# Kernel optimization log

Hardware: AMD Instinct MI355X
Metric: run time of the kernel (lower is better)

The kernel has to match this reference:

```python
import jax, jax.numpy as jnp
import numpy as np

B, S, H, NH = 2, 2048, 1024, 16
D = H // NH
EPS = 1.1920929e-07  # torch fp32 finfo eps used by F.rms_norm default
ROPE_BASE = 10000.0


def setup_inputs() -> dict:
    key = jax.random.key(0)
    k0, k1, k2, k3 = jax.random.split(key, 4)
    return {
        "x": jax.random.normal(k0, (B, S, H), jnp.float32),
        "ve": jax.random.normal(k1, (B, S, H), jnp.float32),
        "W_qkv": jax.random.normal(k2, (3 * H, H), jnp.float32) * 0.02,
        "W_o": jax.random.normal(k3, (H, H), jnp.float32) * 0.02,
        "lambdas": jnp.array([0.5, 0.5], jnp.float32),
    }


def _rms_norm(x):
    # F.rms_norm without learnable weight, over last dim
    return x * jax.lax.rsqrt(jnp.mean(x * x, axis=-1, keepdims=True) + EPS)


def _rope(x):
    # x: [b, s, h, d]; rotate-half style RoPE matching the Rotary module
    d = x.shape[-1]
    inv_freq = (1.0 / ROPE_BASE) ** (jnp.arange(0, d, 2, dtype=jnp.float32) / d)
    t = jnp.arange(x.shape[1], dtype=jnp.float32)
    freqs = t[:, None] * inv_freq[None, :]          # [s, d/2]
    cos = jnp.cos(freqs)[None, :, None, :]
    sin = jnp.sin(freqs)[None, :, None, :]
    x1, x2 = jnp.split(x, 2, axis=-1)
    return jnp.concatenate([x1 * cos + x2 * sin, -x1 * sin + x2 * cos], axis=-1)


def reference(x, ve, W_qkv, W_o, lambdas):
    qkv = x @ W_qkv.T                                # [b, s, 3H]
    q, k, v = jnp.split(qkv, 3, axis=-1)
    rs = lambda a: a.reshape(B, S, NH, D)            # b s (h d) -> b s h d
    q, k, v = rs(q), rs(k), rs(v)
    q = _rope(_rms_norm(q))
    k = _rope(_rms_norm(k))
    v = lambdas[0] * v + lambdas[1] * rs(ve)         # value-lambda mix
    scale = 1.0 / jnp.sqrt(jnp.asarray(D, jnp.float32))  # flex_attention default
    scores = jnp.einsum('bqhd,bkhd->bhqk', q, k) * scale
    causal = jnp.tril(jnp.ones((S, S), bool))
    scores = jnp.where(causal[None, None], scores, jnp.asarray(-jnp.inf, scores.dtype))
    p = jax.nn.softmax(scores, axis=-1)
    a = jnp.einsum('bhqk,bkhd->bqhd', p, v).reshape(B, S, H)
    return a @ W_o.T
```

## Files before the change

kernel.cpp:

```cpp
#include <hip/hip_runtime.h>
#include <math.h>

typedef __bf16 bf16;
typedef __attribute__((ext_vector_type(8))) __bf16 bf16x8;
typedef __attribute__((ext_vector_type(4))) __bf16 bf16x4;
typedef __attribute__((ext_vector_type(4))) float f32x4;

#define B_  2
#define S_  2048
#define H_  1024
#define NH_ 16
#define D_  64

__device__ __forceinline__ f32x4 mfma16(bf16x8 a, bf16x8 b, f32x4 c) {
    return __builtin_amdgcn_mfma_f32_16x16x32_bf16(a, b, c, 0, 0, 0);
}

__device__ __forceinline__ void async16(void* lds, const void* g) {
    __builtin_amdgcn_global_load_lds(
        (const __attribute__((address_space(1))) unsigned int*)g,
        (__attribute__((address_space(3))) unsigned int*)lds, 16, 0, 0);
}

__global__ __launch_bounds__(256) void cvt_main(
    const float* __restrict__ x, const float* __restrict__ wqkv,
    bf16* __restrict__ xb, bf16* __restrict__ wqb, float2* __restrict__ tab)
{
    const int bid = blockIdx.x, tid = threadIdx.x;
    if (bid < 4096) {
        int i = bid * 256 + tid;
        f32x4 v = *(const f32x4*)(x + (size_t)i * 4);
        bf16x4 o; o[0]=(bf16)v[0]; o[1]=(bf16)v[1]; o[2]=(bf16)v[2]; o[3]=(bf16)v[3];
        *(bf16x4*)(xb + (size_t)i * 4) = o;
    } else if (bid < 7168) {
        int i = (bid - 4096) * 256 + tid;
        f32x4 v = *(const f32x4*)(wqkv + (size_t)i * 4);
        bf16x4 o; o[0]=(bf16)v[0]; o[1]=(bf16)v[1]; o[2]=(bf16)v[2]; o[3]=(bf16)v[3];
        *(bf16x4*)(wqb + (size_t)i * 4) = o;
    } else {
        int idx = (bid - 7168) * 256 + tid;
        int s = idx >> 5, i = idx & 31;
        float f = exp2f((float)i * (-13.287712379549449f / 32.0f));
        float sn, cs;
        sincosf((float)s * f, &sn, &cs);
        tab[idx] = make_float2(cs, sn);
    }
}

__global__ __launch_bounds__(256) void cvt_bf16(const float* __restrict__ src,
                                                bf16* __restrict__ dst, int n4) {
    int i = blockIdx.x * 256 + threadIdx.x;
    if (i >= n4) return;
    f32x4 v = *(const f32x4*)(src + (size_t)i * 4);
    bf16x4 o; o[0]=(bf16)v[0]; o[1]=(bf16)v[1]; o[2]=(bf16)v[2]; o[3]=(bf16)v[3];
    *(bf16x4*)(dst + (size_t)i * 4) = o;
}

__global__ __launch_bounds__(512, 2) void gemm_qkv(
    const bf16* __restrict__ A, const bf16* __restrict__ W,
    bf16* __restrict__ qb, bf16* __restrict__ kb, bf16* __restrict__ vtb,
    const float* __restrict__ ve, const float* __restrict__ lambdas,
    const float2* __restrict__ tab)
{
    constexpr int K  = H_;
    constexpr int NS = K >> 6;
    __shared__ bf16 Al[2][256][64];
    __shared__ bf16 Bl[2][256][64];
    const int id = blockIdx.x + 12 * blockIdx.y;
    const int rX = id & 7, qX = id >> 3;
    const int m0 = ((rX >> 2) * 8 + qX / 3) * 256;
    const int n0 = ((rX & 3) * 3 + qX % 3) * 256;
    const int tid  = threadIdx.x;
    const int lane = tid & 63;
    const int w    = tid >> 6;
    const int quad = lane >> 4;
    const int l16  = lane & 15;
    const int l7r  = l16 & 7;
    const int wm   = (w >> 2) * 128;
    const int wn   = (w & 3) * 64;
    const int r8   = lane >> 3;
    const int cs   = ((lane & 7) ^ r8) * 8;

    auto stage_half = [&](int sl, int kt, int h) {
        const int k0 = kt << 6;
        if (h < 2) {
            const bf16* g = A + (size_t)(m0 + h * 128 + w * 16 + r8) * K + k0 + cs;
            async16(&Al[sl][h * 128 + w * 16][0],     g);
            async16(&Al[sl][h * 128 + w * 16 + 8][0], g + (size_t)8 * K);
        } else {
            const bf16* g = W + (size_t)(n0 + (h - 2) * 128 + w * 16 + r8) * K + k0 + cs;
            async16(&Bl[sl][(h - 2) * 128 + w * 16][0],     g);
            async16(&Bl[sl][(h - 2) * 128 + w * 16 + 8][0], g + (size_t)8 * K);
        }
    };

    const f32x4 Z4 = {0.f, 0.f, 0.f, 0.f};
    f32x4 acc[8][4];
#pragma unroll
    for (int i = 0; i < 8; ++i)
#pragma unroll
        for (int j = 0; j < 4; ++j) acc[i][j] = Z4;

    stage_half(0, 0, 0); stage_half(0, 0, 1); stage_half(0, 0, 2); stage_half(0, 0, 3);
    stage_half(1, (NS > 1 ? 1 : 0), 0);

    for (int t = 0; t < NS; ++t) {
        const int cur = t & 1;
        const int kt1 = (t + 1 < NS) ? t + 1 : NS - 1;
        const int kt2 = (t + 2 < NS) ? t + 2 : NS - 1;
        bf16x8 aL[4][2], aH[4][2], bq0[2][2], bq1[2][2];

        asm volatile("s_waitcnt vmcnt(2)" ::: "memory");
        __builtin_amdgcn_s_barrier();
#pragma unroll
        for (int ks = 0; ks < 2; ++ks) {
#pragma unroll
            for (int i = 0; i < 4; ++i)
                aL[i][ks] = *(const bf16x8*)
                    &Al[cur][wm + i * 16 + l16][(((ks << 2) + quad) ^ l7r) * 8];
#pragma unroll
            for (int j = 0; j < 2; ++j)
                bq0[j][ks] = *(const bf16x8*)
                    &Bl[cur][wn + j * 16 + l16][(((ks << 2) + quad) ^ l7r) * 8];
        }
        stage_half(cur ^ 1, kt1, 1);
        __builtin_amdgcn_s_setprio(1);
#pragma unroll
        for (int ks = 0; ks < 2; ++ks)
#pragma unroll
            for (int i = 0; i < 4; ++i)
#pragma unroll
                for (int j = 0; j < 2; ++j)
                    acc[i][j] = mfma16(aL[i][ks], bq0[j][ks], acc[i][j]);
        __builtin_amdgcn_s_setprio(0);

        __builtin_amdgcn_s_barrier();
#pragma unroll
        for (int ks = 0; ks < 2; ++ks)
#pragma unroll
            for (int j = 0; j < 2; ++j)
                bq1[j][ks] = *(const bf16x8*)
                    &Bl[cur][wn + 32 + j * 16 + l16][(((ks << 2) + quad) ^ l7r) * 8];
        stage_half(cur ^ 1, kt1, 2);
        __builtin_amdgcn_s_setprio(1);
#pragma unroll
        for (int ks = 0; ks < 2; ++ks)
#pragma unroll
            for (int i = 0; i < 4; ++i)
#pragma unroll
                for (int j = 0; j < 2; ++j)
                    acc[i][2 + j] = mfma16(aL[i][ks], bq1[j][ks], acc[i][2 + j]);
        __builtin_amdgcn_s_setprio(0);

        __builtin_amdgcn_s_barrier();
#pragma unroll
        for (int ks = 0; ks < 2; ++ks)
#pragma unroll
            for (int i = 0; i < 4; ++i)
                aH[i][ks] = *(const bf16x8*)
                    &Al[cur][wm + 64 + i * 16 + l16][(((ks << 2) + quad) ^ l7r) * 8];
        stage_half(cur ^ 1, kt1, 3);
        __builtin_amdgcn_s_setprio(1);
#pragma unroll
        for (int ks = 0; ks < 2; ++ks)
#pragma unroll
            for (int i = 0; i < 4; ++i)
#pragma unroll
                for (int j = 0; j < 2; ++j)
                    acc[4 + i][j] = mfma16(aH[i][ks], bq0[j][ks], acc[4 + i][j]);
        __builtin_amdgcn_s_setprio(0);

        __builtin_amdgcn_s_barrier();
        stage_half(cur, kt2, 0);
        __builtin_amdgcn_s_setprio(1);
#pragma unroll
        for (int ks = 0; ks < 2; ++ks)
#pragma unroll
            for (int i = 0; i < 4; ++i)
#pragma unroll
                for (int j = 0; j < 2; ++j)
                    acc[4 + i][2 + j] = mfma16(aH[i][ks], bq1[j][ks], acc[4 + i][2 + j]);
        __builtin_amdgcn_s_setprio(0);
    }
    asm volatile("s_waitcnt vmcnt(0)" ::: "memory");

    const int nbase = n0 + wn;
    const int which = nbase >> 10;
    const int h     = (nbase & (H_ - 1)) >> 6;
    if (which < 2) {
        bf16* dst = which ? kb : qb;
#pragma unroll
        for (int i = 0; i < 8; ++i) {
            float ss[4];
#pragma unroll
            for (int r = 0; r < 4; ++r)
                ss[r] = acc[i][0][r] * acc[i][0][r] + acc[i][1][r] * acc[i][1][r]
                      + acc[i][2][r] * acc[i][2][r] + acc[i][3][r] * acc[i][3][r];
#pragma unroll
            for (int r = 0; r < 4; ++r) {
                ss[r] += __shfl_xor(ss[r], 1);
                ss[r] += __shfl_xor(ss[r], 2);
                ss[r] += __shfl_xor(ss[r], 4);
                ss[r] += __shfl_xor(ss[r], 8);
            }
#pragma unroll
            for (int r = 0; r < 4; ++r) {
                int    m   = m0 + wm + i * 16 + quad * 4 + r;
                int    bb  = m >> 11, s = m & (S_ - 1);
                float  rms = rsqrtf(ss[r] * (1.0f / 64.0f) + 1.1920929e-07f);
                float  x0 = acc[i][0][r] * rms, x1 = acc[i][1][r] * rms;
                float  x2 = acc[i][2][r] * rms, x3 = acc[i][3][r] * rms;
                float2 t0 = tab[(size_t)s * 32 + l16];
                float2 t1 = tab[(size_t)s * 32 + 16 + l16];
                bf16*  bp = dst + ((size_t)(bb * NH_ + h) * S_ + s) * D_;
                bp[l16]      = (bf16)(x0 * t0.x + x2 * t0.y);
                bp[16 + l16] = (bf16)(x1 * t1.x + x3 * t1.y);
                bp[32 + l16] = (bf16)(x2 * t0.x - x0 * t0.y);
                bp[48 + l16] = (bf16)(x3 * t1.x - x1 * t1.y);
            }
        }
    } else {
        const float l0 = lambdas[0], l1 = lambdas[1];
#pragma unroll
        for (int i = 0; i < 8; ++i) {
            const int m00 = m0 + wm + i * 16 + quad * 4;
            const int bb  = m00 >> 11, s = m00 & (S_ - 1);
#pragma unroll
            for (int j = 0; j < 4; ++j) {
                const int d = j * 16 + l16;
                bf16x4 pk;
#pragma unroll
                for (int r = 0; r < 4; ++r) {
                    float vm = l0 * acc[i][j][r]
                             + l1 * ve[(size_t)(m00 + r) * H_ + h * 64 + d];
                    pk[r] = (bf16)vm;
                }
                *(bf16x4*)&vtb[((size_t)(bb * NH_ + h) * D_ + d) * S_ + s] = pk;
            }
        }
    }
}

template <int EPI, int NT>
__global__ __launch_bounds__(256) void gemm_bt(
    const bf16* __restrict__ A, const bf16* __restrict__ W,
    int M, int N, int K,
    float* __restrict__ outF)
{
    constexpr int JN = NT / 32;
    __shared__ bf16 Al[128][64];
    __shared__ bf16 Bl[NT][64];
    const int id = blockIdx.x + 16 * blockIdx.y;
    const int rX = id & 7, qX = id >> 3;
    const int m0 = ((rX >> 2) * 16 + (qX >> 2)) * 128;
    const int n0 = ((rX & 3) * 4 + (qX & 3)) * NT;
    const int tid  = threadIdx.x;
    const int lane = tid & 63;
    const int w    = tid >> 6;
    const int quad = lane >> 4;
    const int l16  = lane & 15;
    const int wm   = (w >> 1) * 64;
    const int wn   = (w & 1) * (NT / 2);
    const int r8   = lane >> 3;
    const int cs   = ((lane & 7) ^ r8) * 8;

    const f32x4 Z4 = {0.f, 0.f, 0.f, 0.f};
    f32x4 acc[4][JN];
#pragma unroll
    for (int i = 0; i < 4; ++i)
#pragma unroll
        for (int j = 0; j < JN; ++j) acc[i][j] = Z4;

    for (int k0 = 0; k0 < K; k0 += 64) {
        {
            const bf16* gA = A + (size_t)(m0 + w * 32 + r8) * K + k0 + cs;
            async16(&Al[w * 32][0],      gA);
            async16(&Al[w * 32 + 8][0],  gA + (size_t)8  * K);
            async16(&Al[w * 32 + 16][0], gA + (size_t)16 * K);
            async16(&Al[w * 32 + 24][0], gA + (size_t)24 * K);
        }
        {
            const bf16* gB = W + (size_t)(n0 + w * 16 + r8) * K + k0 + cs;
            async16(&Bl[w * 16][0],     gB);
            async16(&Bl[w * 16 + 8][0], gB + (size_t)8 * K);
        }
        __syncthreads();
#pragma unroll
        for (int ks = 0; ks < 2; ++ks) {
            bf16x8 af[4], bfg[JN];
#pragma unroll
            for (int i = 0; i < 4; ++i)
                af[i] = *(const bf16x8*)
                    &Al[wm + i * 16 + l16][(((ks << 2) + quad) ^ (l16 & 7)) * 8];
#pragma unroll
            for (int j = 0; j < JN; ++j)
                bfg[j] = *(const bf16x8*)
                    &Bl[wn + j * 16 + l16][(((ks << 2) + quad) ^ (l16 & 7)) * 8];
#pragma unroll
            for (int i = 0; i < 4; ++i)
#pragma unroll
                for (int j = 0; j < JN; ++j)
                    acc[i][j] = mfma16(af[i], bfg[j], acc[i][j]);
        }
        __syncthreads();
    }

#pragma unroll
    for (int i = 0; i < 4; ++i)
#pragma unroll
        for (int j = 0; j < JN; ++j)
#pragma unroll
            for (int r = 0; r < 4; ++r) {
                int m = m0 + wm + i * 16 + quad * 4 + r;
                int n = n0 + wn + j * 16 + l16;
                outF[(size_t)m * N + n] = acc[i][j][r];
            }
}

__global__ __launch_bounds__(256) void attn(
    const bf16* __restrict__ Q, const bf16* __restrict__ Kg,
    const bf16* __restrict__ Vt, bf16* __restrict__ Og)
{
    __shared__ bf16 Kl[2][64][64];
    __shared__ bf16 Vl[2][64][64];
    __shared__ bf16 Pl[4][16][64];

    const int id  = blockIdx.x;
    const int xcd = id & 7;
    const int jj  = id >> 3;
    const int sH  = jj & 3;
    const int cC  = jj >> 2;
    const int bh  = xcd + 8 * sH;
    const int c2  = (cC + 16) & 31;
    const int qt  = (sH == 0) ? cC : (sH == 1) ? 31 - cC
                  : (sH == 2) ? c2 : 31 - c2;

    const int b    = bh >> 4;
    const int h    = bh & 15;
    const int tid  = threadIdx.x;
    const int lane = tid & 63;
    const int w    = tid >> 6;
    const int quad = lane >> 4;
    const int l16  = lane & 15;
    const int l7   = l16 & 7;

    const bf16* Qp = Q  + (size_t)bh * S_ * D_;
    const bf16* Kp = Kg + (size_t)bh * S_ * D_;
    const bf16* Vp = Vt + (size_t)bh * D_ * S_;

    const int srow = lane >> 3;
    const int schk = (lane & 7) ^ (lane >> 3);
    const f32x4 Z4 = {0.f, 0.f, 0.f, 0.f};
    const float C1 = 0.18033688011112042f;
    const float C2 = -11.541560327111707f;

    auto stage = [&](int p, int kb0) {
        const bf16* gK = Kp + (size_t)(kb0 + w * 16 + srow) * D_ + schk * 8;
        async16(&Kl[p][w * 16][0], gK);
        async16(&Kl[p][w * 16 + 8][0], gK + (size_t)8 * D_);
        const bf16* gV = Vp + (size_t)(w * 16 + srow) * S_ + kb0 + schk * 8;
        async16(&Vl[p][w * 16][0], gV);
        async16(&Vl[p][w * 16 + 8][0], gV + (size_t)8 * S_);
    };

    const int qbase = qt * 64 + w * 16;
    const int qi    = qbase + l16;

    const bf16x8 qf0 = *(const bf16x8*)(Qp + (size_t)(qbase + l16) * D_ + quad * 8);
    const bf16x8 qf1 = *(const bf16x8*)(Qp + (size_t)(qbase + l16) * D_ + 32 + quad * 8);

    f32x4 of[4];
#pragma unroll
    for (int dt = 0; dt < 4; ++dt) of[dt] = Z4;
    float lsum = 0.f;

    const int nch = qt + 1;
    stage(0, 0);
    for (int c = 0; c < nch; ++c) {
        const int p   = c & 1;
        const int kb0 = c * 64;
        __syncthreads();
        if (c + 1 < nch) stage(p ^ 1, kb0 + 64);

        float ps = 0.f;
        if (c < qt) {
#pragma unroll
            for (int nt = 0; nt < 4; ++nt) {
                bf16x8 kf0 = *(const bf16x8*)&Kl[p][nt * 16 + l16][(quad ^ l7) * 8];
                bf16x8 kf1 = *(const bf16x8*)&Kl[p][nt * 16 + l16][((quad + 4) ^ l7) * 8];
                f32x4 sacc = Z4;
                sacc = mfma16(kf0, qf0, sacc);
                sacc = mfma16(kf1, qf1, sacc);
                bf16x4 pk;
#pragma unroll
                for (int r = 0; r < 4; ++r) {
                    float pv = exp2f(fmaf(sacc[r], C1, C2));
                    ps += pv;
                    pk[r] = (bf16)pv;
                }
                *(bf16x4*)&Pl[w][l16][((nt * 2 + (quad >> 1)) ^ l7) * 8 + (quad & 1) * 4] = pk;
            }
        } else {
#pragma unroll
            for (int nt = 0; nt < 4; ++nt) {
                bf16x8 kf0 = *(const bf16x8*)&Kl[p][nt * 16 + l16][(quad ^ l7) * 8];
                bf16x8 kf1 = *(const bf16x8*)&Kl[p][nt * 16 + l16][((quad + 4) ^ l7) * 8];
                f32x4 sacc = Z4;
                sacc = mfma16(kf0, qf0, sacc);
                sacc = mfma16(kf1, qf1, sacc);
                bf16x4 pk;
#pragma unroll
                for (int r = 0; r < 4; ++r) {
                    int   key = kb0 + nt * 16 + quad * 4 + r;
                    float pv  = (key <= qi) ? exp2f(fmaf(sacc[r], C1, C2)) : 0.f;
                    ps += pv;
                    pk[r] = (bf16)pv;
                }
                *(bf16x4*)&Pl[w][l16][((nt * 2 + (quad >> 1)) ^ l7) * 8 + (quad & 1) * 4] = pk;
            }
        }
        ps += __shfl_xor(ps, 16);
        ps += __shfl_xor(ps, 32);
        lsum += ps;

        bf16x8 pf0 = *(const bf16x8*)&Pl[w][l16][(quad ^ l7) * 8];
        bf16x8 pf1 = *(const bf16x8*)&Pl[w][l16][((quad + 4) ^ l7) * 8];
#pragma unroll
        for (int dt = 0; dt < 4; ++dt) {
            bf16x8 vf0 = *(const bf16x8*)&Vl[p][dt * 16 + l16][(quad ^ l7) * 8];
            bf16x8 vf1 = *(const bf16x8*)&Vl[p][dt * 16 + l16][((quad + 4) ^ l7) * 8];
            of[dt] = mfma16(pf0, vf0, of[dt]);
            of[dt] = mfma16(pf1, vf1, of[dt]);
        }
    }

#pragma unroll
    for (int r = 0; r < 4; ++r) {
        float ld = __shfl(lsum, quad * 4 + r);
        float rl = 1.0f / ld;
        int   qq = qbase + quad * 4 + r;
#pragma unroll
        for (int dt = 0; dt < 4; ++dt)
            Og[((size_t)(b * S_ + qq)) * H_ + h * D_ + dt * 16 + l16] =
                (bf16)(of[dt][r] * rl);
    }
}

extern "C" void kernel_launch(void* const* d_in, const int* in_sizes, int n_in,
                              void* d_out, int out_size, void* d_ws, size_t ws_size,
                              hipStream_t stream)
{
    const float* x       = (const float*)d_in[0];
    const float* ve      = (const float*)d_in[1];
    const float* Wqkv    = (const float*)d_in[2];
    const float* Wo      = (const float*)d_in[3];
    const float* lambdas = (const float*)d_in[4];
    float* out = (float*)d_out;

    char* od = (char*)d_out;
    char* ws = (char*)d_ws;
    const size_t MB = 1024 * 1024;
    bf16*   xb  = (bf16*)(od);
    bf16*   wqb = (bf16*)(od + 8 * MB);
    float2* tab = (float2*)(od + 14 * MB);
    bf16*   qb  = (bf16*)(ws);
    bf16*   kb  = (bf16*)(ws + 8 * MB);
    bf16*   vtb = (bf16*)(ws + 16 * MB);
    bf16*   ao  = (bf16*)(ws + 24 * MB);
    bf16*   wob = (bf16*)(ws);

    cvt_main<<<7424, 256, 0, stream>>>(x, Wqkv, xb, wqb, tab);
    gemm_qkv<<<dim3(12, 16), 512, 0, stream>>>(
        xb, wqb, qb, kb, vtb, ve, lambdas, (const float2*)tab);
    attn<<<dim3(1024), 256, 0, stream>>>(qb, kb, vtb, ao);
    cvt_bf16<<<1024, 256, 0, stream>>>(Wo, wob, (H_ * H_) / 4);
    gemm_bt<1, 64><<<dim3(16, 32), 256, 0, stream>>>(
        ao, wob, B_ * S_, H_, H_, out);
}
```

Baseline: 207.4 us.

## Double-buffer output projection GEMM with async prefetch two stages ahead

Replaces the templated single-buffered output GEMM with a specialized kernel that keeps two LDS stages, prefetching the k-tile two steps ahead while computing the current one. Full __syncthreads pairs become explicit vmcnt waits plus raw barriers, and MFMA sections run under raised wave priority. The goal is to hide global-to-LDS load latency in the final projection. LDS use doubles, and there is a risk from relying on vmcnt counting of the async loads.

```diff
diff --git a/kernel.cpp b/kernel.cpp
--- a/kernel.cpp
+++ b/kernel.cpp
@@ -241,74 +241,93 @@
     }
 }
 
-template <int EPI, int NT>
-__global__ __launch_bounds__(256) void gemm_bt(
+__global__ __launch_bounds__(256) void gemm_o(
     const bf16* __restrict__ A, const bf16* __restrict__ W,
-    int M, int N, int K,
     float* __restrict__ outF)
 {
-    constexpr int JN = NT / 32;
-    __shared__ bf16 Al[128][64];
-    __shared__ bf16 Bl[NT][64];
+    constexpr int K  = H_;
+    constexpr int N  = H_;
+    constexpr int NS = K >> 6;
+    __shared__ bf16 Al[2][128][64];
+    __shared__ bf16 Bl[2][64][64];
     const int id = blockIdx.x + 16 * blockIdx.y;
     const int rX = id & 7, qX = id >> 3;
     const int m0 = ((rX >> 2) * 16 + (qX >> 2)) * 128;
-    const int n0 = ((rX & 3) * 4 + (qX & 3)) * NT;
+    const int n0 = ((rX & 3) * 4 + (qX & 3)) * 64;
     const int tid  = threadIdx.x;
     const int lane = tid & 63;
     const int w    = tid >> 6;
     const int quad = lane >> 4;
     const int l16  = lane & 15;
+    const int l7r  = l16 & 7;
     const int wm   = (w >> 1) * 64;
-    const int wn   = (w & 1) * (NT / 2);
+    const int wn   = (w & 1) * 32;
     const int r8   = lane >> 3;
     const int cs   = ((lane & 7) ^ r8) * 8;
 
+    auto stage = [&](int sl, int k0) {
+        const bf16* gA = A + (size_t)(m0 + w * 32 + r8) * K + k0 + cs;
+        async16(&Al[sl][w * 32][0],      gA);
+        async16(&Al[sl][w * 32 + 8][0],  gA + (size_t)8  * K);
+        async16(&Al[sl][w * 32 + 16][0], gA + (size_t)16 * K);
+        async16(&Al[sl][w * 32 + 24][0], gA + (size_t)24 * K);
+        const bf16* gB = W + (size_t)(n0 + w * 16 + r8) * K + k0 + cs;
+        async16(&Bl[sl][w * 16][0],     gB);
+        async16(&Bl[sl][w * 16 + 8][0], gB + (size_t)8 * K);
+    };
+
     const f32x4 Z4 = {0.f, 0.f, 0.f, 0.f};
-    f32x4 acc[4][JN];
+    f32x4 acc[4][2];
 #pragma unroll
     for (int i = 0; i < 4; ++i)
 #pragma unroll
-        for (int j = 0; j < JN; ++j) acc[i][j] = Z4;
-
-    for (int k0 = 0; k0 < K; k0 += 64) {
-        {
-            const bf16* gA = A + (size_t)(m0 + w * 32 + r8) * K + k0 + cs;
-            async16(&Al[w * 32][0],      gA);
-            async16(&Al[w * 32 + 8][0],  gA + (size_t)8  * K);
-            async16(&Al[w * 32 + 16][0], gA + (size_t)16 * K);
-            async16(&Al[w * 32 + 24][0], gA + (size_t)24 * K);
-        }
-        {
-            const bf16* gB = W + (size_t)(n0 + w * 16 + r8) * K + k0 + cs;
-            async16(&Bl[w * 16][0],     gB);
-            async16(&Bl[w * 16 + 8][0], gB + (size_t)8 * K);
-        }
-        __syncthreads();
+        for (int j = 0; j < 2; ++j) acc[i][j] = Z4;
+
+    stage(0, 0);
+    stage(1, 64);
+
+    for (int t = 0; t < NS; ++t) {
+        const int cur = t & 1;
+        if (t >= NS - 1) { asm volatile("s_waitcnt vmcnt(0)" ::: "memory"); }
+        else             { asm volatile("s_waitcnt vmcnt(6)" ::: "memory"); }
+        __builtin_amdgcn_s_barrier();
+
+        bf16x8 af[4][2], bfg[2][2];
 #pragma unroll
         for (int ks = 0; ks < 2; ++ks) {
-            bf16x8 af[4], bfg[JN];
-#pragma unroll
-            for (int i = 0; i < 4; ++i)
-                af[i] = *(const bf16x8*)
-                    &Al[wm + i * 16 + l16][(((ks << 2) + quad) ^ (l16 & 7)) * 8];
-#pragma unroll
-            for (int j = 0; j < JN; ++j)
-                bfg[j] = *(const bf16x8*)
-                    &Bl[wn + j * 16 + l16][(((ks << 2) + quad) ^ (l16 & 7)) * 8];
-#pragma unroll
-            for (int i = 0; i < 4; ++i)
-#pragma unroll
-                for (int j = 0; j < JN; ++j)
-                    acc[i][j] = mfma16(af[i], bfg[j], acc[i][j]);
-        }
-        __syncthreads();
-    }
+#pragma unroll
+            for (int i = 0; i < 4; ++i)
+                af[i][ks] = *(const bf16x8*)
+                    &Al[cur][wm + i * 16 + l16][(((ks << 2) + quad) ^ l7r) * 8];
+#pragma unroll
+            for (int j = 0; j < 2; ++j)
+                bfg[j][ks] = *(const bf16x8*)
+                    &Bl[cur][wn + j * 16 + l16][(((ks << 2) + quad) ^ l7r) * 8];
+        }
+        __builtin_amdgcn_s_setprio(1);
+#pragma unroll
+        for (int i = 0; i < 4; ++i)
+#pragma unroll
+            for (int j = 0; j < 2; ++j)
+                acc[i][j] = mfma16(af[i][0], bfg[j][0], acc[i][j]);
+        __builtin_amdgcn_s_setprio(0);
+
+        __builtin_amdgcn_s_barrier();
+        if (t + 2 < NS) stage(cur, (t + 2) << 6);
+        __builtin_amdgcn_s_setprio(1);
+#pragma unroll
+        for (int i = 0; i < 4; ++i)
+#pragma unroll
+            for (int j = 0; j < 2; ++j)
+                acc[i][j] = mfma16(af[i][1], bfg[j][1], acc[i][j]);
+        __builtin_amdgcn_s_setprio(0);
+    }
+    asm volatile("s_waitcnt vmcnt(0)" ::: "memory");
 
 #pragma unroll
     for (int i = 0; i < 4; ++i)
 #pragma unroll
-        for (int j = 0; j < JN; ++j)
+        for (int j = 0; j < 2; ++j)
 #pragma unroll
             for (int r = 0; r < 4; ++r) {
                 int m = m0 + wm + i * 16 + quad * 4 + r;
@@ -474,6 +493,5 @@
         xb, wqb, qb, kb, vtb, ve, lambdas, (const float2*)tab);
     attn<<<dim3(1024), 256, 0, stream>>>(qb, kb, vtb, ao);
     cvt_bf16<<<1024, 256, 0, stream>>>(Wo, wob, (H_ * H_) / 4);
-    gemm_bt<1, 64><<<dim3(16, 32), 256, 0, stream>>>(
-        ao, wob, B_ * S_, H_, H_, out);
-}
+    gemm_o<<<dim3(16, 32), 256, 0, stream>>>(ao, wob, out);
+}
```

Result: faster. 201.6 us (-2.8%).
